# Kernel tuning notes

Hardware: AMD Instinct MI355X
Metric: run time of the kernel (lower is better)

The kernel has to match this reference:

```python
import jax, jax.numpy as jnp
import numpy as np

T, D, H, E, K = 8192, 1024, 1024, 8, 2
N = T * K  # total dispatched rows


def setup_inputs() -> dict:
    key = jax.random.key(0)
    ks = jax.random.split(key, 12)
    s = 1.0 / np.sqrt(D)
    inp = {
        # uniform, contiguous per-expert segments: 2048 rows each
        'offsets': jnp.arange(E + 1, dtype=jnp.int64 if jax.config.jax_enable_x64 else jnp.int32) * (N // E),
        'jagged': jax.random.normal(ks[0], (T, D), jnp.float32),
        'weight': jax.random.normal(ks[1], (E, D, H), jnp.float32) * s,
        'bias': jax.random.normal(ks[2], (E, H), jnp.float32) * 0.02,
        'index': jax.random.randint(ks[3], (N,), 0, T),
        'weight_p': jax.random.normal(ks[4], (E, D, H), jnp.float32) * s,
        'weight_out': jax.random.normal(ks[5], (E, H, D), jnp.float32) * (1.0 / np.sqrt(H)),
        'reverse_index': jax.random.randint(ks[6], (T, K), 0, N),
        'gates': jax.random.uniform(ks[7], (N,), jnp.float32),
        'gates_index': jax.random.randint(ks[8], (T, K), 0, N),
        'bias_p': jax.random.normal(ks[9], (E, H), jnp.float32) * 0.02,
        'bias_out': jax.random.normal(ks[10], (E, D), jnp.float32) * 0.02,
    }
    return inp


def reference(offsets, jagged, weight, bias, index, weight_p, weight_out,
              reverse_index, gates, gates_index, bias_p, bias_out):
    # dispatch: gather token features into expert-sorted order  [N, D]
    x = jagged[index]
    n = x.shape[0]
    n_experts = weight.shape[0]
    # contiguous segment id per dispatched row
    expert_id = jnp.searchsorted(offsets, jnp.arange(n), side='right') - 1
    y = jnp.zeros((n, weight_out.shape[-1]), dtype=x.dtype)
    for e in range(n_experts):  # fixed small expert count
        m = (expert_id == e)[:, None].astype(x.dtype)
        xe = x * m
        g = xe @ weight[e] + bias[e]        # gate proj  [N, H]
        u = xe @ weight_p[e] + bias_p[e]    # up proj    [N, H]
        h = jax.nn.silu(g) * u              # SwiGLU
        y = y + (h @ weight_out[e] + bias_out[e]) * m
    # combine: gather K expert outputs per token, weight by gates  [T, D]
    gathered = y[reverse_index]             # [T, K, D]
    gv = gates[gates_index]                 # [T, K]
    return jnp.einsum('tkd,tk->td', gathered, gv)
```

## Files before the change

kernel.cpp:

```cpp
#include <hip/hip_runtime.h>
#include <hip/hip_bf16.h>

#define T_TOK 8192
#define DDIM 1024
#define HDIM 1024
#define NEXP 8
#define KTOP 2
#define NROWS (T_TOK * KTOP)

typedef __attribute__((ext_vector_type(8))) short bf16x8;
typedef __attribute__((ext_vector_type(8))) unsigned short u16x8;
typedef __attribute__((ext_vector_type(4))) float f32x4;

__device__ __forceinline__ unsigned short f2bf(float f) {
    unsigned u = __builtin_bit_cast(unsigned, f);
    u += 0x7fffu + ((u >> 16) & 1u);
    return (unsigned short)(u >> 16);
}
__device__ __forceinline__ float bf2f(unsigned short h) {
    return __builtin_bit_cast(float, (unsigned)h << 16);
}

__device__ __forceinline__ void gll16(const unsigned short* g, const unsigned short* l) {
    __builtin_amdgcn_global_load_lds(
        (const __attribute__((address_space(1))) unsigned int*)g,
        (__attribute__((address_space(3))) unsigned int*)l, 16, 0, 0);
}


__global__ __launch_bounds__(256) void cvt_bf16_k(const float* __restrict__ in,
                                                  unsigned short* __restrict__ out, int n4) {
    int i = blockIdx.x * 256 + threadIdx.x;
    if (i >= n4) return;
    float4 v = ((const float4*)in)[i];
    ushort4 o;
    o.x = f2bf(v.x); o.y = f2bf(v.y); o.z = f2bf(v.z); o.w = f2bf(v.w);
    ((ushort4*)out)[i] = o;
}

__global__ __launch_bounds__(256) void transpose_cast3_k(
    const float* __restrict__ w1, const float* __restrict__ w2,
    const float* __restrict__ w3, unsigned short* __restrict__ o1,
    unsigned short* __restrict__ o2, unsigned short* __restrict__ o3) {
    __shared__ float tile[64][65];
    int z = blockIdx.z;
    int which = z >> 3, m = z & 7;
    const float* src = (which == 0 ? w1 : which == 1 ? w2 : w3) + (size_t)m * DDIM * HDIM;
    unsigned short* dst = (which == 0 ? o1 : which == 1 ? o2 : o3) + (size_t)m * DDIM * HDIM;
    int c0 = blockIdx.x * 64, r0 = blockIdx.y * 64;
    int t = threadIdx.x;
    int rr = t >> 4;
    int cc = (t & 15) * 4;
#pragma unroll
    for (int p = 0; p < 4; ++p) {
        float4 v = *(const float4*)&src[(size_t)(r0 + rr + p * 16) * HDIM + c0 + cc];
        tile[rr + p * 16][cc]     = v.x;
        tile[rr + p * 16][cc + 1] = v.y;
        tile[rr + p * 16][cc + 2] = v.z;
        tile[rr + p * 16][cc + 3] = v.w;
    }
    __syncthreads();
    int rb = (t & 7) * 8;
    int oc = t >> 3;
#pragma unroll
    for (int q = 0; q < 2; ++q) {
        int c = oc + q * 32;
        u16x8 o;
#pragma unroll
        for (int j = 0; j < 8; ++j)
            o[j] = f2bf(tile[rb + j][c]);
        *(u16x8*)&dst[(size_t)(c0 + c) * DDIM + r0 + rb] = o;
    }
}


constexpr int BMk = 128, BNk = 128, BKk = 64;

__global__ __launch_bounds__(256, 2) void gemm128_fused_k(
    const unsigned short* __restrict__ A, const int* __restrict__ rowidx,
    const unsigned short* __restrict__ B1t, const unsigned short* __restrict__ B2t,
    const float* __restrict__ b1E, const float* __restrict__ b2E,
    unsigned short* __restrict__ Out, const int* __restrict__ offsets) {
    const int N = HDIM, K = DDIM, lda = DDIM;
    __shared__ __attribute__((aligned(16))) unsigned short lds[24576];

    const int nbn = N / BNk;
    int l = (blockIdx.x & 7) * 128 + (blockIdx.x >> 3);
    int brow = l / nbn, bcol = l % nbn;
    int row0 = brow * BMk, col0 = bcol * BNk;
    int e = 0;
    while (offsets[e + 1] <= row0) ++e;

    const unsigned short* B1e = B1t + (size_t)e * N * K;
    const unsigned short* B2e = B2t + (size_t)e * N * K;
    const float* b1 = b1E + (size_t)e * N;
    const float* b2 = b2E + (size_t)e * N;

    int tid = threadIdx.x;
    int lane = tid & 63, wid = tid >> 6;
    int wr = wid >> 1, wc = wid & 1;
    int l15 = lane & 15, l4 = lane >> 4;

    int srow = lane >> 3;
    int c8 = ((lane & 7) ^ srow) * 8;
    const unsigned short* aS[4];
    const unsigned short* b1S[4];
    const unsigned short* b2S[4];
#pragma unroll
    for (int q = 0; q < 4; ++q) {
        int g = wid * 4 + q;
        int gr = row0 + g * 8 + srow;
        aS[q]  = A + (size_t)rowidx[gr] * lda + c8;
        b1S[q] = B1e + (size_t)(col0 + g * 8 + srow) * K + c8;
        b2S[q] = B2e + (size_t)(col0 + g * 8 + srow) * K + c8;
    }

    const char* LB = (const char*)lds;
    int arow = (wr * 64 + l15) * 128;
    int brw = (wc * 64 + l15) * 128;
    int cx = l15 & 7;
    int ch0 = (l4 ^ cx) * 16;
    int ch1 = ((4 + l4) ^ cx) * 16;

    f32x4 acc1[4][4] = {};
    f32x4 acc2[4][4] = {};

#pragma unroll 1
    for (int t = 0; t < K / BKk; ++t) {
        int k0 = t * BKk;
#pragma unroll
        for (int q = 0; q < 4; ++q) {
            gll16(aS[q] + k0,  lds + (wid * 4 + q) * 512);
            gll16(b1S[q] + k0, lds + 8192 + (wid * 4 + q) * 512);
            gll16(b2S[q] + k0, lds + 16384 + (wid * 4 + q) * 512);
        }
        __syncthreads();
#pragma unroll
        for (int s = 0; s < 2; ++s) {
            int ch = s ? ch1 : ch0;
            bf16x8 fa[4], fb1[4], fb2[4];
#pragma unroll
            for (int mi = 0; mi < 4; ++mi)
                fa[mi] = *(const bf16x8*)(LB + arow + mi * 2048 + ch);
#pragma unroll
            for (int ni = 0; ni < 4; ++ni) {
                fb1[ni] = *(const bf16x8*)(LB + 8192 * 2 + brw + ni * 2048 + ch);
                fb2[ni] = *(const bf16x8*)(LB + 8192 * 4 + brw + ni * 2048 + ch);
            }
#pragma unroll
            for (int mi = 0; mi < 4; ++mi)
#pragma unroll
                for (int ni = 0; ni < 4; ++ni) {
                    acc1[mi][ni] = __builtin_amdgcn_mfma_f32_16x16x32_bf16(
                        fa[mi], fb1[ni], acc1[mi][ni], 0, 0, 0);
                    acc2[mi][ni] = __builtin_amdgcn_mfma_f32_16x16x32_bf16(
                        fa[mi], fb2[ni], acc2[mi][ni], 0, 0, 0);
                }
        }
        __syncthreads();
    }

    float bv1[4], bv2[4];
#pragma unroll
    for (int ni = 0; ni < 4; ++ni) {
        int c = col0 + wc * 64 + ni * 16 + l15;
        bv1[ni] = b1[c];
        bv2[ni] = b2[c];
    }

#pragma unroll
    for (int mi = 0; mi < 4; ++mi) {
        int orow_b = row0 + wr * 64 + mi * 16 + l4 * 4;
#pragma unroll
        for (int ni = 0; ni < 4; ++ni) {
            int ocol = col0 + wc * 64 + ni * 16 + l15;
#pragma unroll
            for (int q = 0; q < 4; ++q) {
                float g = acc1[mi][ni][q] + bv1[ni];
                float u = acc2[mi][ni][q] + bv2[ni];
                float s = g / (1.0f + __expf(-g));
                Out[(size_t)(orow_b + q) * N + ocol] = f2bf(s * u);
            }
        }
    }
}


__global__ __launch_bounds__(256, 2) void gemm128_dualrow_k(
    const unsigned short* __restrict__ A, int lda,
    const unsigned short* __restrict__ Bt, const float* __restrict__ biasE,
    unsigned short* __restrict__ Out, const int* __restrict__ offsets,
    int N, int K) {
    __shared__ __attribute__((aligned(16))) unsigned short lds[24576];

    const int nbn = N / BNk;
    int l = (blockIdx.x & 7) * 64 + (blockIdx.x >> 3);
    int brow = l / nbn, bcol = l % nbn;
    int row0 = brow * 256, col0 = bcol * BNk;
    int e = 0;
    while (offsets[e + 1] <= row0) ++e;

    const unsigned short* Bte = Bt + (size_t)e * N * K;
    const float* bias = biasE + (size_t)e * N;

    int tid = threadIdx.x;
    int lane = tid & 63, wid = tid >> 6;
    int wr = wid >> 1, wc = wid & 1;
    int l15 = lane & 15, l4 = lane >> 4;

    int srow = lane >> 3;
    int c8 = ((lane & 7) ^ srow) * 8;
    const unsigned short* a1S[4];
    const unsigned short* a2S[4];
    const unsigned short* bS[4];
#pragma unroll
    for (int q = 0; q < 4; ++q) {
        int g = wid * 4 + q;
        a1S[q] = A + (size_t)(row0 + g * 8 + srow) * lda + c8;
        a2S[q] = A + (size_t)(row0 + 128 + g * 8 + srow) * lda + c8;
        bS[q]  = Bte + (size_t)(col0 + g * 8 + srow) * K + c8;
    }

    const char* LB = (const char*)lds;
    int arow = (wr * 64 + l15) * 128;
    int brw = (wc * 64 + l15) * 128;
    int cx = l15 & 7;
    int ch0 = (l4 ^ cx) * 16;
    int ch1 = ((4 + l4) ^ cx) * 16;

    f32x4 acc1[4][4] = {};
    f32x4 acc2[4][4] = {};

#pragma unroll 1
    for (int t = 0; t < K / BKk; ++t) {
        int k0 = t * BKk;
#pragma unroll
        for (int q = 0; q < 4; ++q) {
            gll16(a1S[q] + k0, lds + (wid * 4 + q) * 512);
            gll16(a2S[q] + k0, lds + 8192 + (wid * 4 + q) * 512);
            gll16(bS[q] + k0,  lds + 16384 + (wid * 4 + q) * 512);
        }
        __syncthreads();
#pragma unroll
        for (int s = 0; s < 2; ++s) {
            int ch = s ? ch1 : ch0;
            bf16x8 fa1[4], fa2[4], fb[4];
#pragma unroll
            for (int mi = 0; mi < 4; ++mi) {
                fa1[mi] = *(const bf16x8*)(LB + arow + mi * 2048 + ch);
                fa2[mi] = *(const bf16x8*)(LB + 16384 + arow + mi * 2048 + ch);
            }
#pragma unroll
            for (int ni = 0; ni < 4; ++ni)
                fb[ni] = *(const bf16x8*)(LB + 32768 + brw + ni * 2048 + ch);
#pragma unroll
            for (int mi = 0; mi < 4; ++mi)
#pragma unroll
                for (int ni = 0; ni < 4; ++ni) {
                    acc1[mi][ni] = __builtin_amdgcn_mfma_f32_16x16x32_bf16(
                        fa1[mi], fb[ni], acc1[mi][ni], 0, 0, 0);
                    acc2[mi][ni] = __builtin_amdgcn_mfma_f32_16x16x32_bf16(
                        fa2[mi], fb[ni], acc2[mi][ni], 0, 0, 0);
                }
        }
        __syncthreads();
    }

    float bv[4];
#pragma unroll
    for (int ni = 0; ni < 4; ++ni)
        bv[ni] = bias[col0 + wc * 64 + ni * 16 + l15];

#pragma unroll
    for (int mi = 0; mi < 4; ++mi) {
        int orow1 = row0 + wr * 64 + mi * 16 + l4 * 4;
        int orow2 = orow1 + 128;
#pragma unroll
        for (int ni = 0; ni < 4; ++ni) {
            int ocol = col0 + wc * 64 + ni * 16 + l15;
#pragma unroll
            for (int q = 0; q < 4; ++q) {
                Out[(size_t)(orow1 + q) * N + ocol] = f2bf(acc1[mi][ni][q] + bv[ni]);
                Out[(size_t)(orow2 + q) * N + ocol] = f2bf(acc2[mi][ni][q] + bv[ni]);
            }
        }
    }
}


__global__ __launch_bounds__(256) void combine_k(
    const unsigned short* __restrict__ Y, const int* __restrict__ rev,
    const float* __restrict__ gates, const int* __restrict__ gidx,
    float* __restrict__ out) {
    int t = blockIdx.x;
    int r0 = rev[2 * t], r1 = rev[2 * t + 1];
    float g0 = gates[gidx[2 * t]], g1 = gates[gidx[2 * t + 1]];
    const unsigned short* y0 = Y + (size_t)r0 * DDIM;
    const unsigned short* y1 = Y + (size_t)r1 * DDIM;
    int d = threadIdx.x * 4;
    ushort4 a = *(const ushort4*)(y0 + d);
    ushort4 b = *(const ushort4*)(y1 + d);
    float4 r;
    r.x = g0 * bf2f(a.x) + g1 * bf2f(b.x);
    r.y = g0 * bf2f(a.y) + g1 * bf2f(b.y);
    r.z = g0 * bf2f(a.z) + g1 * bf2f(b.z);
    r.w = g0 * bf2f(a.w) + g1 * bf2f(b.w);
    *(float4*)(out + (size_t)t * DDIM + d) = r;
}


extern "C" void kernel_launch(void* const* d_in, const int* in_sizes, int n_in,
                              void* d_out, int out_size, void* d_ws, size_t ws_size,
                              hipStream_t stream) {
    const int* offsets = (const int*)d_in[0];
    const float* jagged = (const float*)d_in[1];
    const float* weight = (const float*)d_in[2];
    const float* bias = (const float*)d_in[3];
    const int* index = (const int*)d_in[4];
    const float* weight_p = (const float*)d_in[5];
    const float* weight_out = (const float*)d_in[6];
    const int* rev = (const int*)d_in[7];
    const float* gates = (const float*)d_in[8];
    const int* gidx = (const int*)d_in[9];
    const float* bias_p = (const float*)d_in[10];
    const float* bias_out = (const float*)d_in[11];
    float* out = (float*)d_out;

    char* w = (char*)d_ws;
    unsigned short* jag_bf = (unsigned short*)w; w += (size_t)T_TOK * DDIM * 2;
    unsigned short* W1t    = (unsigned short*)w; w += (size_t)NEXP * DDIM * HDIM * 2;
    unsigned short* Wpt    = (unsigned short*)w; w += (size_t)NEXP * DDIM * HDIM * 2;
    unsigned short* Wot    = (unsigned short*)w; w += (size_t)NEXP * HDIM * DDIM * 2;
    unsigned short* h_ws   = (unsigned short*)w; w += (size_t)NROWS * HDIM * 2;
    unsigned short* y_ws   = (unsigned short*)w; w += (size_t)NROWS * DDIM * 2;

    cvt_bf16_k<<<(T_TOK * DDIM / 4 + 255) / 256, 256, 0, stream>>>(jagged, jag_bf, T_TOK * DDIM / 4);
    transpose_cast3_k<<<dim3(HDIM / 64, DDIM / 64, 3 * NEXP), 256, 0, stream>>>(
        weight, weight_p, weight_out, W1t, Wpt, Wot);

    const int grid = (NROWS / BMk) * (HDIM / BNk);

    gemm128_fused_k<<<grid, 256, 0, stream>>>(jag_bf, index, W1t, Wpt, bias, bias_p,
                                              h_ws, offsets);
    const int grid_y = (NROWS / 256) * (DDIM / BNk);
    gemm128_dualrow_k<<<grid_y, 256, 0, stream>>>(h_ws, HDIM, Wot, bias_out, y_ws,
                                                  offsets, DDIM, HDIM);
    combine_k<<<T_TOK, 256, 0, stream>>>(y_ws, rev, gates, gidx, out);
}
```

Measured before the change: 155.0 us.

## Load weight MFMA fragments directly from global memory instead of LDS staging

Both expert GEMM kernels no longer stage the weight (B) tiles through shared memory. Each lane now reads its bf16x8 B fragments straight from global memory into registers, while activations still go through LDS. This shrinks LDS use and removes the global-to-LDS copy and LDS reads for B. In exchange, each wave fetches B separately from global/L2 with uncoalesced 16-byte loads that are not shared across the waves of a block, and these loads sit on the critical path without prefetch.

New measurement: 241.4 us. +55.7%, slower.

```diff
diff --git a/kernel.cpp b/kernel.cpp
--- a/kernel.cpp
+++ b/kernel.cpp
@@ -82,7 +82,7 @@
     const float* __restrict__ b1E, const float* __restrict__ b2E,
     unsigned short* __restrict__ Out, const int* __restrict__ offsets) {
     const int N = HDIM, K = DDIM, lda = DDIM;
-    __shared__ __attribute__((aligned(16))) unsigned short lds[24576];
+    __shared__ __attribute__((aligned(16))) unsigned short lds[8192];
 
     const int nbn = N / BNk;
     int l = (blockIdx.x & 7) * 128 + (blockIdx.x >> 3);
@@ -104,20 +104,23 @@
     int srow = lane >> 3;
     int c8 = ((lane & 7) ^ srow) * 8;
     const unsigned short* aS[4];
-    const unsigned short* b1S[4];
-    const unsigned short* b2S[4];
 #pragma unroll
     for (int q = 0; q < 4; ++q) {
-        int g = wid * 4 + q;
-        int gr = row0 + g * 8 + srow;
-        aS[q]  = A + (size_t)rowidx[gr] * lda + c8;
-        b1S[q] = B1e + (size_t)(col0 + g * 8 + srow) * K + c8;
-        b2S[q] = B2e + (size_t)(col0 + g * 8 + srow) * K + c8;
+        int gr = row0 + (wid * 4 + q) * 8 + srow;
+        aS[q] = A + (size_t)rowidx[gr] * lda + c8;
+    }
+
+    const unsigned short* b1P[4];
+    const unsigned short* b2P[4];
+#pragma unroll
+    for (int ni = 0; ni < 4; ++ni) {
+        int c = col0 + wc * 64 + ni * 16 + l15;
+        b1P[ni] = B1e + (size_t)c * K + l4 * 8;
+        b2P[ni] = B2e + (size_t)c * K + l4 * 8;
     }
 
     const char* LB = (const char*)lds;
     int arow = (wr * 64 + l15) * 128;
-    int brw = (wc * 64 + l15) * 128;
     int cx = l15 & 7;
     int ch0 = (l4 ^ cx) * 16;
     int ch1 = ((4 + l4) ^ cx) * 16;
@@ -129,23 +132,21 @@
     for (int t = 0; t < K / BKk; ++t) {
         int k0 = t * BKk;
 #pragma unroll
-        for (int q = 0; q < 4; ++q) {
-            gll16(aS[q] + k0,  lds + (wid * 4 + q) * 512);
-            gll16(b1S[q] + k0, lds + 8192 + (wid * 4 + q) * 512);
-            gll16(b2S[q] + k0, lds + 16384 + (wid * 4 + q) * 512);
-        }
+        for (int q = 0; q < 4; ++q)
+            gll16(aS[q] + k0, lds + (wid * 4 + q) * 512);
         __syncthreads();
 #pragma unroll
         for (int s = 0; s < 2; ++s) {
             int ch = s ? ch1 : ch0;
+            int kk = k0 + s * 32;
             bf16x8 fa[4], fb1[4], fb2[4];
 #pragma unroll
             for (int mi = 0; mi < 4; ++mi)
                 fa[mi] = *(const bf16x8*)(LB + arow + mi * 2048 + ch);
 #pragma unroll
             for (int ni = 0; ni < 4; ++ni) {
-                fb1[ni] = *(const bf16x8*)(LB + 8192 * 2 + brw + ni * 2048 + ch);
-                fb2[ni] = *(const bf16x8*)(LB + 8192 * 4 + brw + ni * 2048 + ch);
+                fb1[ni] = *(const bf16x8*)(b1P[ni] + kk);
+                fb2[ni] = *(const bf16x8*)(b2P[ni] + kk);
             }
 #pragma unroll
             for (int mi = 0; mi < 4; ++mi)
@@ -191,7 +192,7 @@
     const unsigned short* __restrict__ Bt, const float* __restrict__ biasE,
     unsigned short* __restrict__ Out, const int* __restrict__ offsets,
     int N, int K) {
-    __shared__ __attribute__((aligned(16))) unsigned short lds[24576];
+    __shared__ __attribute__((aligned(16))) unsigned short lds[16384];
 
     const int nbn = N / BNk;
     int l = (blockIdx.x & 7) * 64 + (blockIdx.x >> 3);
@@ -212,18 +213,22 @@
     int c8 = ((lane & 7) ^ srow) * 8;
     const unsigned short* a1S[4];
     const unsigned short* a2S[4];
-    const unsigned short* bS[4];
 #pragma unroll
     for (int q = 0; q < 4; ++q) {
         int g = wid * 4 + q;
         a1S[q] = A + (size_t)(row0 + g * 8 + srow) * lda + c8;
         a2S[q] = A + (size_t)(row0 + 128 + g * 8 + srow) * lda + c8;
-        bS[q]  = Bte + (size_t)(col0 + g * 8 + srow) * K + c8;
+    }
+
+    const unsigned short* bP[4];
+#pragma unroll
+    for (int ni = 0; ni < 4; ++ni) {
+        int c = col0 + wc * 64 + ni * 16 + l15;
+        bP[ni] = Bte + (size_t)c * K + l4 * 8;
     }
 
     const char* LB = (const char*)lds;
     int arow = (wr * 64 + l15) * 128;
-    int brw = (wc * 64 + l15) * 128;
     int cx = l15 & 7;
     int ch0 = (l4 ^ cx) * 16;
     int ch1 = ((4 + l4) ^ cx) * 16;
@@ -238,12 +243,12 @@
         for (int q = 0; q < 4; ++q) {
             gll16(a1S[q] + k0, lds + (wid * 4 + q) * 512);
             gll16(a2S[q] + k0, lds + 8192 + (wid * 4 + q) * 512);
-            gll16(bS[q] + k0,  lds + 16384 + (wid * 4 + q) * 512);
         }
         __syncthreads();
 #pragma unroll
         for (int s = 0; s < 2; ++s) {
             int ch = s ? ch1 : ch0;
+            int kk = k0 + s * 32;
             bf16x8 fa1[4], fa2[4], fb[4];
 #pragma unroll
             for (int mi = 0; mi < 4; ++mi) {
@@ -252,7 +257,7 @@
             }
 #pragma unroll
             for (int ni = 0; ni < 4; ++ni)
-                fb[ni] = *(const bf16x8*)(LB + 32768 + brw + ni * 2048 + ch);
+                fb[ni] = *(const bf16x8*)(bP[ni] + kk);
 #pragma unroll
             for (int mi = 0; mi < 4; ++mi)
 #pragma unroll
```

## Double-buffer two of three LDS operand tiles to overlap loads with MFMA

Applied to the files above, without the earlier changes.

Both GEMM kernels now prefetch the next K-tile for two of the three operands into alternate LDS buffers while the current tile is being computed. The third operand stays single-buffered and is loaded after compute, which needs an extra barrier. LDS per block grows from 48 KB to 80 KB to hide global-load latency behind MFMA work. The cost is a second __syncthreads per iteration, a serialized third-operand load, and possibly lower occupancy, since two blocks would need 160 KB of LDS.

Result: slower. 158.3 us (+2.1%).

```diff
diff --git a/kernel.cpp b/kernel.cpp
--- a/kernel.cpp
+++ b/kernel.cpp
@@ -82,7 +82,7 @@
     const float* __restrict__ b1E, const float* __restrict__ b2E,
     unsigned short* __restrict__ Out, const int* __restrict__ offsets) {
     const int N = HDIM, K = DDIM, lda = DDIM;
-    __shared__ __attribute__((aligned(16))) unsigned short lds[24576];
+    __shared__ __attribute__((aligned(16))) unsigned short lds[40960];
 
     const int nbn = N / BNk;
     int l = (blockIdx.x & 7) * 128 + (blockIdx.x >> 3);
@@ -115,6 +115,13 @@
         b2S[q] = B2e + (size_t)(col0 + g * 8 + srow) * K + c8;
     }
 
+#define STG_A(T)  { int _b = (T) & 1; _Pragma("unroll") for (int q = 0; q < 4; ++q) \
+        gll16(aS[q] + (T) * BKk, lds + _b * 8192 + (wid * 4 + q) * 512); }
+#define STG_B1(T) { int _b = (T) & 1; _Pragma("unroll") for (int q = 0; q < 4; ++q) \
+        gll16(b1S[q] + (T) * BKk, lds + 16384 + _b * 8192 + (wid * 4 + q) * 512); }
+#define STG_B2(T) { _Pragma("unroll") for (int q = 0; q < 4; ++q) \
+        gll16(b2S[q] + (T) * BKk, lds + 32768 + (wid * 4 + q) * 512); }
+
     const char* LB = (const char*)lds;
     int arow = (wr * 64 + l15) * 128;
     int brw = (wc * 64 + l15) * 128;
@@ -125,27 +132,26 @@
     f32x4 acc1[4][4] = {};
     f32x4 acc2[4][4] = {};
 
+    STG_A(0) STG_B1(0) STG_B2(0)
+    __syncthreads();
+
 #pragma unroll 1
     for (int t = 0; t < K / BKk; ++t) {
-        int k0 = t * BKk;
-#pragma unroll
-        for (int q = 0; q < 4; ++q) {
-            gll16(aS[q] + k0,  lds + (wid * 4 + q) * 512);
-            gll16(b1S[q] + k0, lds + 8192 + (wid * 4 + q) * 512);
-            gll16(b2S[q] + k0, lds + 16384 + (wid * 4 + q) * 512);
-        }
-        __syncthreads();
+        if (t + 1 < K / BKk) { STG_A(t + 1) STG_B1(t + 1) }
+        const char* Ab  = LB + (t & 1) * 16384;
+        const char* B1b = LB + 32768 + (t & 1) * 16384;
+        const char* B2b = LB + 65536;
 #pragma unroll
         for (int s = 0; s < 2; ++s) {
             int ch = s ? ch1 : ch0;
             bf16x8 fa[4], fb1[4], fb2[4];
 #pragma unroll
             for (int mi = 0; mi < 4; ++mi)
-                fa[mi] = *(const bf16x8*)(LB + arow + mi * 2048 + ch);
+                fa[mi] = *(const bf16x8*)(Ab + arow + mi * 2048 + ch);
 #pragma unroll
             for (int ni = 0; ni < 4; ++ni) {
-                fb1[ni] = *(const bf16x8*)(LB + 8192 * 2 + brw + ni * 2048 + ch);
-                fb2[ni] = *(const bf16x8*)(LB + 8192 * 4 + brw + ni * 2048 + ch);
+                fb1[ni] = *(const bf16x8*)(B1b + brw + ni * 2048 + ch);
+                fb2[ni] = *(const bf16x8*)(B2b + brw + ni * 2048 + ch);
             }
 #pragma unroll
             for (int mi = 0; mi < 4; ++mi)
@@ -158,7 +164,12 @@
                 }
         }
         __syncthreads();
-    }
+        if (t + 1 < K / BKk) STG_B2(t + 1)
+        __syncthreads();
+    }
+#undef STG_A
+#undef STG_B1
+#undef STG_B2
 
     float bv1[4], bv2[4];
 #pragma unroll
@@ -191,7 +202,7 @@
     const unsigned short* __restrict__ Bt, const float* __restrict__ biasE,
     unsigned short* __restrict__ Out, const int* __restrict__ offsets,
     int N, int K) {
-    __shared__ __attribute__((aligned(16))) unsigned short lds[24576];
+    __shared__ __attribute__((aligned(16))) unsigned short lds[40960];
 
     const int nbn = N / BNk;
     int l = (blockIdx.x & 7) * 64 + (blockIdx.x >> 3);
@@ -221,6 +232,13 @@
         bS[q]  = Bte + (size_t)(col0 + g * 8 + srow) * K + c8;
     }
 
+#define STG_A1(T) { int _b = (T) & 1; _Pragma("unroll") for (int q = 0; q < 4; ++q) \
+        gll16(a1S[q] + (T) * BKk, lds + _b * 8192 + (wid * 4 + q) * 512); }
+#define STG_A2(T) { int _b = (T) & 1; _Pragma("unroll") for (int q = 0; q < 4; ++q) \
+        gll16(a2S[q] + (T) * BKk, lds + 16384 + _b * 8192 + (wid * 4 + q) * 512); }
+#define STG_B(T)  { _Pragma("unroll") for (int q = 0; q < 4; ++q) \
+        gll16(bS[q] + (T) * BKk, lds + 32768 + (wid * 4 + q) * 512); }
+
     const char* LB = (const char*)lds;
     int arow = (wr * 64 + l15) * 128;
     int brw = (wc * 64 + l15) * 128;
@@ -231,28 +249,27 @@
     f32x4 acc1[4][4] = {};
     f32x4 acc2[4][4] = {};
 
+    STG_A1(0) STG_A2(0) STG_B(0)
+    __syncthreads();
+
 #pragma unroll 1
     for (int t = 0; t < K / BKk; ++t) {
-        int k0 = t * BKk;
-#pragma unroll
-        for (int q = 0; q < 4; ++q) {
-            gll16(a1S[q] + k0, lds + (wid * 4 + q) * 512);
-            gll16(a2S[q] + k0, lds + 8192 + (wid * 4 + q) * 512);
-            gll16(bS[q] + k0,  lds + 16384 + (wid * 4 + q) * 512);
-        }
-        __syncthreads();
+        if (t + 1 < K / BKk) { STG_A1(t + 1) STG_A2(t + 1) }
+        const char* A1b = LB + (t & 1) * 16384;
+        const char* A2b = LB + 32768 + (t & 1) * 16384;
+        const char* Bb  = LB + 65536;
 #pragma unroll
         for (int s = 0; s < 2; ++s) {
             int ch = s ? ch1 : ch0;
             bf16x8 fa1[4], fa2[4], fb[4];
 #pragma unroll
             for (int mi = 0; mi < 4; ++mi) {
-                fa1[mi] = *(const bf16x8*)(LB + arow + mi * 2048 + ch);
-                fa2[mi] = *(const bf16x8*)(LB + 16384 + arow + mi * 2048 + ch);
+                fa1[mi] = *(const bf16x8*)(A1b + arow + mi * 2048 + ch);
+                fa2[mi] = *(const bf16x8*)(A2b + arow + mi * 2048 + ch);
             }
 #pragma unroll
             for (int ni = 0; ni < 4; ++ni)
-                fb[ni] = *(const bf16x8*)(LB + 32768 + brw + ni * 2048 + ch);
+                fb[ni] = *(const bf16x8*)(Bb + brw + ni * 2048 + ch);
 #pragma unroll
             for (int mi = 0; mi < 4; ++mi)
 #pragma unroll
@@ -264,7 +281,12 @@
                 }
         }
         __syncthreads();
-    }
+        if (t + 1 < K / BKk) STG_B(t + 1)
+        __syncthreads();
+    }
+#undef STG_A1
+#undef STG_A2
+#undef STG_B
 
     float bv[4];
 #pragma unroll
```
